# Performance work log

Measured on AMD Instinct MI355X. Metric: run time of the kernel, lower is better.

Reference implementation:

```python
import jax, jax.numpy as jnp
import numpy as np

NEG = -1e18


def _split_heads(x, h):
    # [B, L, D] -> [B, H, L, D/H]
    b, l, d = x.shape
    return x.reshape(b, l, h, d // h).transpose(0, 2, 1, 3)


def _merge_heads(x):
    # [B, H, L, Dh] -> [B, L, H*Dh]
    b, h, l, dh = x.shape
    return x.transpose(0, 2, 1, 3).reshape(b, l, h * dh)


def _sparse(att, dp_map):
    # att: [B, H, L] per-token scores; dp_map: [B, 2, L] (row, col) tree indices.
    # scatter att[b,h,t] -> S[b, h, dp_map[b,0,t], dp_map[b,1,t]], then symmetrize.
    B, H, L = att.shape
    bi = jnp.arange(B)[:, None, None]          # [B,1,1]
    hi = jnp.arange(H)[None, :, None]          # [1,H,1]
    p0 = dp_map[:, 0, :][:, None, :]           # [B,1,L]
    p1 = dp_map[:, 1, :][:, None, :]           # [B,1,L]
    s = jnp.zeros((B, H, L, L), att.dtype)
    s = s.at[bi, hi, p0, p1].set(att)          # matches torch index_put_ (overwrite)
    return s + jnp.swapaxes(s, 2, 3)


def _reverse(values, dp_map):
    # r[b, j] = values[b, dp_map[b,0,j]] for j >= 1; r[b,0] = 0
    idx = dp_map[:, 0, :]                      # [B, L]
    r = jnp.take_along_axis(values, idx[:, :, None], axis=1)
    return r.at[:, 0, :].set(0.0)


def setup_inputs() -> dict:
    key = jax.random.key(0)
    ks = jax.random.split(key, 16)
    B, L, D, R, H = 16, 384, 768, 768, 12
    inp = {
        "queries":   jax.random.normal(ks[0], (B, L, D), jnp.float32),
        "keys":      jax.random.normal(ks[1], (B, L, D), jnp.float32),
        "values":    jax.random.normal(ks[2], (B, L, D), jnp.float32),
        "relations": jax.random.normal(ks[3], (B, L, R), jnp.float32),
        "dp_map":    jax.random.randint(ks[4], (B, 2, L), 0, L, jnp.int32),
        "mask":      jax.random.bernoulli(ks[5], 0.1, (B, L, L)),
        "rel_mask":  jax.random.bernoulli(ks[6], 0.1, (B, L, 1)),
        "Wq":  jax.random.normal(ks[7],  (D, D), jnp.float32) * 0.02,
        "Wk":  jax.random.normal(ks[8],  (D, D), jnp.float32) * 0.02,
        "Wv":  jax.random.normal(ks[9],  (D, D), jnp.float32) * 0.02,
        "Wo":  jax.random.normal(ks[10], (D, D), jnp.float32) * 0.02,
        "Wge": jax.random.normal(ks[11], (D, R), jnp.float32) * 0.02,
        "Wgr": jax.random.normal(ks[12], (R, R), jnp.float32) * 0.02,
        "Vr":  jax.random.normal(ks[13], (R, 1), jnp.float32) * 0.02,
        "Vg":  jax.random.normal(ks[14], (R, 1), jnp.float32) * 0.02,
    }
    return inp


def reference(queries, keys, values, relations, dp_map, mask, rel_mask,
              Wq, Wk, Wv, Wo, Wge, Wgr, Vr, Vg):
    H = 12
    R = Vg.shape[0]
    Dk = Wq.shape[1]
    scale = (Dk // H) ** -0.5

    # config.is_reverse = True path
    hv = jnp.where(rel_mask, 0.0, _reverse(values, dp_map))       # [B,L,D]
    rel = jnp.where(rel_mask, 0.0, relations)                     # [B,L,R]

    # semantic gated mechanism
    rv_h = _split_heads(rel @ Wgr, H)                             # [B,H,L,R/H]
    hs_h = _split_heads(hv @ Wge, H)
    Vg_h = Vg.reshape(H, R // H, 1)
    g = jnp.tanh(jnp.einsum('bhld,hdo->bhlo', hs_h + rv_h, Vg_h))[..., 0]
    gated = _sparse(g, dp_map)                                    # [B,H,L,L]

    q = _split_heads(queries @ Wq, H) * scale
    k = _split_heads(keys @ Wk, H)
    v = _split_heads(values @ Wv, H)
    rel_h = _split_heads(rel, H)
    Vr_h = Vr.reshape(H, R // H, 1)

    self_logits = jnp.einsum('bhqd,bhkd->bhqk', q, k)             # [B,H,L,L]
    rel_logits = _sparse(jnp.einsum('bhld,hdo->bhlo', rel_h, Vr_h)[..., 0], dp_map)

    m = mask[:, None]                                             # [B,1,L,L]
    self_logits = jnp.where(m, NEG, self_logits)
    rel_logits = jnp.where(m, NEG, rel_logits)

    attention_weights = self_logits.sum(axis=1) / H               # [B,L,L]
    sw = jax.nn.softmax(self_logits, axis=-1)
    rw = jax.nn.softmax(rel_logits, axis=-1)
    w = (1.0 - gated) * sw + gated * rw                           # dropout p=0

    ctx = jnp.einsum('bhqk,bhkd->bhqd', w, v)
    out = _merge_heads(ctx) @ Wo
    return out, attention_weights
```

## Files before the change

kernel.cpp:

```cpp
#include <hip/hip_runtime.h>
#include <math.h>

#define Bn 16
#define Lq 384
#define Hn 12
#define Dm 768
#define DH 64
#define QT2 16
#define NEGV (-1e18f)
#define SPADU 404

typedef __attribute__((ext_vector_type(4))) float f32x4;
typedef __attribute__((ext_vector_type(8))) __bf16 bf16x8;
typedef __attribute__((ext_vector_type(4))) __bf16 bf16x4;
typedef unsigned short ushort_t;
typedef unsigned int uint_t;

__device__ __forceinline__ ushort_t f2b(float f) {
  unsigned int u = __float_as_uint(f);
  unsigned int r = (u + 0x7FFFu + ((u >> 16) & 1u)) >> 16;
  return (ushort_t)r;
}
__device__ __forceinline__ float b2f(ushort_t u) {
  return __uint_as_float(((unsigned int)u) << 16);
}
__device__ __forceinline__ bf16x8 cvt8(float4 a, float4 b) {
  bf16x8 r;
  r[0] = (__bf16)a.x; r[1] = (__bf16)a.y; r[2] = (__bf16)a.z; r[3] = (__bf16)a.w;
  r[4] = (__bf16)b.x; r[5] = (__bf16)b.y; r[6] = (__bf16)b.z; r[7] = (__bf16)b.w;
  return r;
}

__global__ __launch_bounds__(256) void k_prep(
    const float* __restrict__ Wge, const float* __restrict__ Wgr,
    const float* __restrict__ Vg,
    float* __restrict__ Age, float* __restrict__ Agr,
    const float* __restrict__ W0, const float* __restrict__ W1,
    const float* __restrict__ W2, const float* __restrict__ W3,
    ushort_t* __restrict__ T0, ushort_t* __restrict__ T1,
    ushort_t* __restrict__ T2, ushort_t* __restrict__ T3,
    const int* __restrict__ dp, int* __restrict__ win)
{
  __shared__ float vg[DH];
  __shared__ float t[32][33];
  int blk = blockIdx.x;
  if (blk < 24) {
    int which = blk / Hn;
    int h = blk % Hn;
    const float* Wsrc = which ? Wgr : Wge;
    float* dst = which ? Agr : Age;
    if (threadIdx.x < DH) vg[threadIdx.x] = Vg[h*DH + threadIdx.x];
    __syncthreads();
    for (int d = threadIdx.x; d < Dm; d += 256) {
      const float* wrow = Wsrc + (size_t)d*Dm + h*DH;
      float s = 0.f;
      #pragma unroll 8
      for (int j = 0; j < DH; ++j) s = fmaf(wrow[j], vg[j], s);
      dst[h*Dm + d] = s;
    }
  } else if (blk < 24 + 2304) {
    int b2 = blk - 24;
    int z = b2 / 576, rem = b2 % 576;
    const float* W = (z == 0) ? W0 : (z == 1) ? W1 : (z == 2) ? W2 : W3;
    ushort_t* WT = (z == 0) ? T0 : (z == 1) ? T1 : (z == 2) ? T2 : T3;
    int k0 = (rem / 24)*32, n0 = (rem % 24)*32;
    int tx = threadIdx.x & 31, ty = threadIdx.x >> 5;
    #pragma unroll
    for (int r = 0; r < 4; ++r)
      t[ty + r*8][tx] = W[(size_t)(k0 + ty + r*8)*Dm + n0 + tx];
    __syncthreads();
    #pragma unroll
    for (int r = 0; r < 4; ++r)
      WT[(size_t)(n0 + ty + r*8)*Dm + k0 + tx] = f2b(t[tx][ty + r*8]);
  } else {
    int i = (blk - 2328)*256 + threadIdx.x;
    int b = i / Lq, l = i % Lq;
    int p0 = dp[(size_t)(b*2+0)*Lq + l];
    int p1 = dp[(size_t)(b*2+1)*Lq + l];
    atomicMax(&win[(size_t)b*Lq*Lq + (size_t)p0*Lq + p1], l);
  }
}

__global__ __launch_bounds__(256) void k_pair(
    const int* __restrict__ win, const int* __restrict__ mask,
    uint_t* __restrict__ wpair)
{
  __shared__ int tB[32][33];
  int b = blockIdx.z;
  int i0 = blockIdx.x*32, j0 = blockIdx.y*32;
  const int* wb = win + (size_t)b*Lq*Lq;
  const int* mb = mask + (size_t)b*Lq*Lq;
  int tx = threadIdx.x & 31, ty = threadIdx.x >> 5;
  #pragma unroll
  for (int rr = 0; rr < 4; ++rr) {
    int r = ty + rr*8;
    tB[r][tx] = wb[(size_t)(j0+r)*Lq + i0 + tx];
  }
  __syncthreads();
  #pragma unroll
  for (int rr = 0; rr < 4; ++rr) {
    int ti = ty + rr*8;
    int i = i0 + ti, j = j0 + tx;
    int l1 = wb[(size_t)i*Lq + j];
    int l2 = tB[tx][ti];
    int mk = mb[(size_t)i*Lq + j];
    wpair[(size_t)b*Lq*Lq + (size_t)i*Lq + j] =
        ((uint_t)(mk != 0) << 31) | ((unsigned)(l1 + 1) << 16) | (unsigned)(l2 + 1);
  }
}

__global__ __launch_bounds__(256) void k_grlog(
    const float* __restrict__ values, const float* __restrict__ relations,
    const int* __restrict__ dp, const int* __restrict__ rel_mask,
    const float* __restrict__ Age, const float* __restrict__ Agr,
    const float* __restrict__ Vr,
    float* __restrict__ g, float* __restrict__ rlog)
{
  int blk = blockIdx.x;
  int b = blk / (Lq/4), l0 = (blk % (Lq/4))*4;
  int tid = threadIdx.x, lane = tid & 63, wave = tid >> 6;
  __shared__ float relrow[4][Dm], hvrow[4][Dm];
  #pragma unroll
  for (int rr = 0; rr < 4; ++rr) {
    int l = l0 + rr;
    int rm = rel_mask[(size_t)b*Lq + l];
    int idx = dp[(size_t)(b*2)*Lq + l];
    const float* vrow = values + ((size_t)b*Lq + idx)*Dm;
    const float* rrow = relations + ((size_t)b*Lq + l)*Dm;
    for (int d = tid; d < Dm; d += 256) {
      relrow[rr][d] = rm ? 0.f : rrow[d];
      hvrow[rr][d]  = (rm || l == 0) ? 0.f : vrow[d];
    }
  }
  __syncthreads();
  int l = l0 + wave;
  for (int h = 0; h < Hn; ++h) {
    float p = 0.f;
    #pragma unroll
    for (int k = 0; k < Dm/64; ++k) {
      int d = lane + 64*k;
      p = fmaf(hvrow[wave][d], Age[h*Dm + d],
          fmaf(relrow[wave][d], Agr[h*Dm + d], p));
    }
    #pragma unroll
    for (int o = 32; o > 0; o >>= 1) p += __shfl_xor(p, o);
    if (lane == 0) g[((size_t)b*Hn + h)*Lq + l] = tanhf(p);
  }
  if (lane < Hn) {
    float s = 0.f;
    #pragma unroll 8
    for (int j = 0; j < DH; ++j)
      s = fmaf(relrow[wave][lane*DH + j], Vr[lane*DH + j], s);
    rlog[((size_t)b*Hn + lane)*Lq + l] = s;
  }
}

__global__ __launch_bounds__(256) void k_mmqkv(
    const float* __restrict__ Xq, const float* __restrict__ Xk,
    const float* __restrict__ Xv,
    const ushort_t* __restrict__ WqT, const ushort_t* __restrict__ WkT,
    const ushort_t* __restrict__ WvT,
    ushort_t* __restrict__ qbf, ushort_t* __restrict__ kbf,
    ushort_t* __restrict__ vTbf)
{
  const int K = Dm;
  __shared__ ushort_t As[128*64];
  __shared__ ushort_t Bs[128*64];

  int z = blockIdx.z;
  const float* A     = (z == 0) ? Xq : (z == 1) ? Xk : Xv;
  const ushort_t* BT = (z == 0) ? WqT : (z == 1) ? WkT : WvT;

  int bm = blockIdx.x;
  int bn = blockIdx.y;
  int m_blk = bm*128;

  int t = threadIdx.x;
  int wave = t >> 6, lane = t & 63;
  int wr = wave >> 1, wc = wave & 1;
  int lrow = lane & 15, lkg = lane >> 4;

  f32x4 acc[4][4];
  #pragma unroll
  for (int i = 0; i < 4; ++i)
    #pragma unroll
    for (int j = 0; j < 4; ++j) acc[i][j] = (f32x4)(0.f);

  int sr = t >> 3, sc8 = t & 7;
  for (int k0 = 0; k0 < K; k0 += 64) {
    __syncthreads();
    #pragma unroll
    for (int i = 0; i < 4; ++i) {
      int row = sr + i*32;
      const float* ap = A + (size_t)(m_blk + row)*K + k0 + sc8*8;
      float4 f0 = *(const float4*)ap;
      float4 f1 = *(const float4*)(ap + 4);
      uint4 vb = *(const uint4*)(BT + (size_t)(bn*128 + row)*K + k0 + sc8*8);
      int slot = sc8 ^ (row & 7);
      *(bf16x8*)&As[row*64 + slot*8] = cvt8(f0, f1);
      *(uint4*)&Bs[row*64 + slot*8] = vb;
    }
    __syncthreads();
    #pragma unroll
    for (int kk = 0; kk < 2; ++kk) {
      bf16x8 aF[4], bF[4];
      int chunk = kk*4 + lkg;
      #pragma unroll
      for (int mi = 0; mi < 4; ++mi) {
        int arow = wr*64 + mi*16 + lrow;
        aF[mi] = *(const bf16x8*)&As[arow*64 + ((chunk ^ (arow & 7)) << 3)];
        int brow = wc*64 + mi*16 + lrow;
        bF[mi] = *(const bf16x8*)&Bs[brow*64 + ((chunk ^ (brow & 7)) << 3)];
      }
      #pragma unroll
      for (int mi = 0; mi < 4; ++mi)
        #pragma unroll
        for (int ni = 0; ni < 4; ++ni)
          acc[mi][ni] = __builtin_amdgcn_mfma_f32_16x16x32_bf16(
              aF[mi], bF[ni], acc[mi][ni], 0, 0, 0);
    }
  }

  float alpha = (z == 0) ? 0.125f : 1.f;
  #pragma unroll
  for (int mi = 0; mi < 4; ++mi) {
    #pragma unroll
    for (int ni = 0; ni < 4; ++ni) {
      f32x4 a = acc[mi][ni];
      int rit = wr*64 + mi*16 + 4*lkg;
      int cit = wc*64 + ni*16 + lrow;
      int gcol = bn*128 + cit;
      if (z < 2) {
        ushort_t* Cb = z ? kbf : qbf;
        int grow = m_blk + rit;
        #pragma unroll
        for (int r = 0; r < 4; ++r)
          Cb[(size_t)(grow + r)*Dm + gcol] = f2b(a[r]*alpha);
      } else {
        int b = bm/3;
        int rl = (bm%3)*128 + rit;
        ushort4 u;
        u.x = f2b(a[0]); u.y = f2b(a[1]); u.z = f2b(a[2]); u.w = f2b(a[3]);
        *(ushort4*)&vTbf[((size_t)b*Dm + gcol)*Lq + rl] = u;
      }
    }
  }
}

template<int MODE>
__global__ __launch_bounds__(256) void k_mm64(
    const ushort_t* __restrict__ A, const ushort_t* __restrict__ BT,
    float* __restrict__ Cf, const int* __restrict__ mask, float alpha)
{
  const int K = Dm;
  __shared__ ushort_t As[64*64];
  __shared__ ushort_t Bs[128*64];

  int bm = blockIdx.x, bn = blockIdx.y, b = blockIdx.z;
  const ushort_t* Ab = (MODE == 3) ? A  + (size_t)b*Lq*Dm : A;
  const ushort_t* Bb = (MODE == 3) ? BT + (size_t)b*Lq*Dm : BT;
  int m0 = bm*64, n0 = bn*128;

  int t = threadIdx.x;
  int wave = t >> 6, lane = t & 63;
  int wr = wave >> 1, wc = wave & 1;
  int lrow = lane & 15, lkg = lane >> 4;

  f32x4 acc[2][4];
  #pragma unroll
  for (int i = 0; i < 2; ++i)
    #pragma unroll
    for (int j = 0; j < 4; ++j) acc[i][j] = (f32x4)(0.f);

  int sr = t >> 3, sc8 = t & 7;
  for (int k0 = 0; k0 < K; k0 += 64) {
    __syncthreads();
    #pragma unroll
    for (int i = 0; i < 2; ++i) {
      int row = sr + i*32;
      uint4 va = *(const uint4*)(Ab + (size_t)(m0 + row)*K + k0 + sc8*8);
      int slot = sc8 ^ (row & 7);
      *(uint4*)&As[row*64 + slot*8] = va;
    }
    #pragma unroll
    for (int i = 0; i < 4; ++i) {
      int row = sr + i*32;
      uint4 vb = *(const uint4*)(Bb + (size_t)(n0 + row)*K + k0 + sc8*8);
      int slot = sc8 ^ (row & 7);
      *(uint4*)&Bs[row*64 + slot*8] = vb;
    }
    __syncthreads();
    #pragma unroll
    for (int kk = 0; kk < 2; ++kk) {
      bf16x8 aF[2], bF[4];
      int chunk = kk*4 + lkg;
      #pragma unroll
      for (int mi = 0; mi < 2; ++mi) {
        int arow = wr*32 + mi*16 + lrow;
        aF[mi] = *(const bf16x8*)&As[arow*64 + ((chunk ^ (arow & 7)) << 3)];
      }
      #pragma unroll
      for (int ni = 0; ni < 4; ++ni) {
        int brow = wc*64 + ni*16 + lrow;
        bF[ni] = *(const bf16x8*)&Bs[brow*64 + ((chunk ^ (brow & 7)) << 3)];
      }
      #pragma unroll
      for (int mi = 0; mi < 2; ++mi)
        #pragma unroll
        for (int ni = 0; ni < 4; ++ni)
          acc[mi][ni] = __builtin_amdgcn_mfma_f32_16x16x32_bf16(
              aF[mi], bF[ni], acc[mi][ni], 0, 0, 0);
    }
  }

  #pragma unroll
  for (int mi = 0; mi < 2; ++mi) {
    #pragma unroll
    for (int ni = 0; ni < 4; ++ni) {
      f32x4 a = acc[mi][ni];
      int rit = wr*32 + mi*16 + 4*lkg;
      int cit = wc*64 + ni*16 + lrow;
      if (MODE == 0) {
        int grow = m0 + rit, gcol = n0 + cit;
        #pragma unroll
        for (int r = 0; r < 4; ++r)
          Cf[(size_t)(grow + r)*Dm + gcol] = a[r]*alpha;
      } else {
        int rl = m0 + rit, cl = n0 + cit;
        const int* mb2 = mask + (size_t)b*Lq*Lq;
        float* awb = Cf + (size_t)b*Lq*Lq;
        #pragma unroll
        for (int r = 0; r < 4; ++r) {
          int m = mb2[(size_t)(rl + r)*Lq + cl];
          awb[(size_t)(rl + r)*Lq + cl] = m ? NEGV : a[r]*alpha;
        }
      }
    }
  }
}

__global__ __launch_bounds__(256, 8) void k_attn3(
    const ushort_t* __restrict__ qbf, const ushort_t* __restrict__ kbf,
    const ushort_t* __restrict__ vT, const uint_t* __restrict__ wpair,
    const float* __restrict__ g, const float* __restrict__ rlog,
    ushort_t* __restrict__ ctxbf)
{
  __shared__ ushort_t S16[QT2][SPADU];
  __shared__ float2 rg2[Lq + 1];

  int bid = blockIdx.x;
  int h  = bid % Hn;
  int qt = (bid / Hn) % (Lq/QT2);
  int b  = bid / (Hn * (Lq/QT2));
  int q0 = qt * QT2;
  int tid = threadIdx.x, lane = tid & 63, wave = tid >> 6;
  int lrow = lane & 15, lkg = lane >> 4;
  int w4 = wave*4;

  const uint_t* wpb = wpair + (size_t)b*Lq*Lq;
  const float* gh = g    + ((size_t)b*Hn + h)*Lq;
  const float* rh = rlog + ((size_t)b*Hn + h)*Lq;

  uint_t wpre[4][6];
  #pragma unroll
  for (int r = 0; r < 4; ++r) {
    const uint_t* wrow = wpb + (size_t)(q0 + w4 + r)*Lq + lane;
    #pragma unroll
    for (int u = 0; u < 6; ++u) wpre[r][u] = wrow[u*64];
  }

  if (tid == 0) { rg2[0].x = 0.f; rg2[0].y = 0.f; }
  for (int e = tid; e < Lq; e += 256) {
    float2 v2; v2.x = rh[e]; v2.y = gh[e];
    rg2[e + 1] = v2;
  }

  {
    const ushort_t* qb = qbf + ((size_t)b*Lq + q0 + lrow)*Dm + h*DH + lkg*8;
    bf16x8 aF0 = *(const bf16x8*)(qb);
    bf16x8 aF1 = *(const bf16x8*)(qb + 32);
    int col0 = wave*96;
    #pragma unroll
    for (int tt = 0; tt < 6; ++tt) {
      int col = col0 + tt*16 + lrow;
      const ushort_t* kb = kbf + ((size_t)b*Lq + col)*Dm + h*DH + lkg*8;
      bf16x8 bF0 = *(const bf16x8*)(kb);
      bf16x8 bF1 = *(const bf16x8*)(kb + 32);
      f32x4 z = (f32x4)(0.f);
      z = __builtin_amdgcn_mfma_f32_16x16x32_bf16(aF0, bF0, z, 0, 0, 0);
      z = __builtin_amdgcn_mfma_f32_16x16x32_bf16(aF1, bF1, z, 0, 0, 0);
      #pragma unroll
      for (int r = 0; r < 4; ++r)
        S16[4*lkg + r][col] = f2b(__expf(z[r]));
    }
  }
  __syncthreads();

  for (int r = 0; r < 4; ++r) {
    int row = w4 + r;
    float sv[6], rv[6], gv[6];
    float ssum = 0.f, rsum = 0.f;
    #pragma unroll
    for (int u = 0; u < 6; ++u) {
      int kj = u*64 + lane;
      uint_t w = wpre[r][u];
      uint_t i1 = (w >> 16) & 0x7FFFu;
      uint_t i2 = w & 0xFFFFu;
      float2 a = rg2[i1];
      float2 c = rg2[i2];
      bool msk = (int)w < 0;
      sv[u] = msk ? 0.f : b2f(S16[row][kj]);
      rv[u] = msk ? 0.f : __expf(a.x + c.x);
      gv[u] = a.y + c.y;
      ssum += sv[u]; rsum += rv[u];
    }
    #pragma unroll
    for (int o = 32; o > 0; o >>= 1) {
      ssum += __shfl_xor(ssum, o);
      rsum += __shfl_xor(rsum, o);
    }
    float si = 1.f/ssum, ri = 1.f/rsum;
    ushort_t* prow = &S16[row][0];
    #pragma unroll
    for (int u = 0; u < 6; ++u) {
      int kj = u*64 + lane;
      float t1 = sv[u]*si;
      float p = fmaf(gv[u], fmaf(rv[u], ri, -t1), t1);
      prow[kj] = f2b(p);
    }
  }
  __syncthreads();

  {
    int dcol = h*DH + wave*16 + lrow;
    const ushort_t* vb = vT + ((size_t)b*Dm + dcol)*Lq + lkg*8;
    const ushort_t* prow = &S16[lrow][0];
    f32x4 o = (f32x4)(0.f);
    #pragma unroll
    for (int ks = 0; ks < 12; ++ks) {
      bf16x4 lo = *(const bf16x4*)(prow + ks*32 + lkg*8);
      bf16x4 hi = *(const bf16x4*)(prow + ks*32 + lkg*8 + 4);
      bf16x8 pa = __builtin_shufflevector(lo, hi, 0,1,2,3,4,5,6,7);
      bf16x8 bv = *(const bf16x8*)(vb + ks*32);
      o = __builtin_amdgcn_mfma_f32_16x16x32_bf16(pa, bv, o, 0, 0, 0);
    }
    #pragma unroll
    for (int r = 0; r < 4; ++r)
      ctxbf[((size_t)b*Lq + q0 + 4*lkg + r)*Dm + dcol] = f2b(o[r]);
  }
}

extern "C" void kernel_launch(void* const* d_in, const int* in_sizes, int n_in,
                              void* d_out, int out_size, void* d_ws, size_t ws_size,
                              hipStream_t stream) {
  const float* queries   = (const float*)d_in[0];
  const float* keys      = (const float*)d_in[1];
  const float* values    = (const float*)d_in[2];
  const float* relations = (const float*)d_in[3];
  const int*   dp_map    = (const int*)d_in[4];
  const int*   mask      = (const int*)d_in[5];
  const int*   rel_mask  = (const int*)d_in[6];
  const float* Wq  = (const float*)d_in[7];
  const float* Wk  = (const float*)d_in[8];
  const float* Wv  = (const float*)d_in[9];
  const float* Wo  = (const float*)d_in[10];
  const float* Wge = (const float*)d_in[11];
  const float* Wgr = (const float*)d_in[12];
  const float* Vr  = (const float*)d_in[13];
  const float* Vg  = (const float*)d_in[14];

  float* ws = (float*)d_ws;
  const size_t SZ   = (size_t)Bn*Lq*Dm;
  const size_t WINS = (size_t)Bn*Lq*Lq;
  const size_t GSZ  = (size_t)Bn*Hn*Lq;

  int*   win  = (int*)ws;
  float* g    = ws + WINS;
  float* rlog = g + GSZ;
  float* Age  = rlog + GSZ;
  float* Agr  = Age + (size_t)Hn*Dm;
  uint_t* wpair = (uint_t*)(Agr + (size_t)Hn*Dm);
  ushort_t* p0 = (ushort_t*)(wpair + WINS);
  ushort_t* qbf  = p0;
  ushort_t* kbf  = p0 + SZ;
  ushort_t* vTbf = p0 + 2*SZ;
  ushort_t* ctxbf= p0 + 3*SZ;
  ushort_t* WqT  = p0 + 4*SZ;
  ushort_t* WkT  = WqT + (size_t)Dm*Dm;
  ushort_t* WvT  = WkT + (size_t)Dm*Dm;
  ushort_t* WoT  = WvT + (size_t)Dm*Dm;

  float* outp = (float*)d_out;
  float* awp  = outp + SZ;

  hipMemsetAsync(win, 0xFF, WINS*sizeof(int), stream);
  k_prep<<<2352, 256, 0, stream>>>(Wge, Wgr, Vg, Age, Agr,
                                   Wq, Wk, Wv, Wo, WqT, WkT, WvT, WoT,
                                   dp_map, win);
  k_grlog<<<Bn*Lq/4, 256, 0, stream>>>(values, relations, dp_map, rel_mask,
                                       Age, Agr, Vr, g, rlog);
  k_mmqkv<<<dim3(48, 6, 3), 256, 0, stream>>>(queries, keys, values,
                                              WqT, WkT, WvT, qbf, kbf, vTbf);
  k_pair<<<dim3(Lq/32, Lq/32, Bn), 256, 0, stream>>>(win, mask, wpair);
  k_mm64<3><<<dim3(6, 3, Bn), 256, 0, stream>>>(qbf, kbf, awp, mask, 1.f/12.f);
  k_attn3<<<Bn*(Lq/QT2)*Hn, 256, 0, stream>>>(qbf, kbf, vTbf, wpair, g, rlog,
                                              ctxbf);
  k_mm64<0><<<dim3(96, 6, 1), 256, 0, stream>>>(ctxbf, WoT, outp, nullptr, 1.f);
}
```

Measured before the change: 197.3 us.

## Replace dense pair map with mask bitsets and sparse per-row relation entries

Replaces the dense per-element wpair array, which k_attn3 read for every (q,k) pair, with a 64-bit mask bitset per row plus a compact per-row list of tree-index entries capped at ECAP. The relation softmax sum is computed as the count of unmasked positions plus corrections from the sparse entries, and only those entries get their probabilities patched. This cuts a large global read in the attention kernel and the wpair write. In exchange it adds atomics in the collect pass and silently drops entries if a row has more than ECAP nonzeros.

Result: slower. 226.2 us (+14.7%).

```diff
diff --git a/kernel.cpp b/kernel.cpp
--- a/kernel.cpp
+++ b/kernel.cpp
@@ -9,12 +9,14 @@
 #define QT2 16
 #define NEGV (-1e18f)
 #define SPADU 404
+#define ECAP 32
 
 typedef __attribute__((ext_vector_type(4))) float f32x4;
 typedef __attribute__((ext_vector_type(8))) __bf16 bf16x8;
 typedef __attribute__((ext_vector_type(4))) __bf16 bf16x4;
 typedef unsigned short ushort_t;
 typedef unsigned int uint_t;
+typedef unsigned long long ull_t;
 
 __device__ __forceinline__ ushort_t f2b(float f) {
   unsigned int u = __float_as_uint(f);
@@ -39,7 +41,8 @@
     const float* __restrict__ W2, const float* __restrict__ W3,
     ushort_t* __restrict__ T0, ushort_t* __restrict__ T1,
     ushort_t* __restrict__ T2, ushort_t* __restrict__ T3,
-    const int* __restrict__ dp, int* __restrict__ win)
+    const int* __restrict__ dp, int* __restrict__ win,
+    const int* __restrict__ mask, ull_t* __restrict__ mbits)
 {
   __shared__ float vg[DH];
   __shared__ float t[32][33];
@@ -72,24 +75,39 @@
     #pragma unroll
     for (int r = 0; r < 4; ++r)
       WT[(size_t)(n0 + ty + r*8)*Dm + k0 + tx] = f2b(t[tx][ty + r*8]);
-  } else {
+  } else if (blk < 2352) {
     int i = (blk - 2328)*256 + threadIdx.x;
     int b = i / Lq, l = i % Lq;
     int p0 = dp[(size_t)(b*2+0)*Lq + l];
     int p1 = dp[(size_t)(b*2+1)*Lq + l];
     atomicMax(&win[(size_t)b*Lq*Lq + (size_t)p0*Lq + p1], l);
-  }
-}
-
-__global__ __launch_bounds__(256) void k_pair(
-    const int* __restrict__ win, const int* __restrict__ mask,
-    uint_t* __restrict__ wpair)
+  } else {
+    int rr = blk - 2352;
+    int lane = threadIdx.x & 63, wave = threadIdx.x >> 6;
+    int gi = rr*4 + wave;
+    const int* mrow = mask + (size_t)gi*Lq;
+    ull_t w0 = __ballot(mrow[lane]        != 0);
+    ull_t w1 = __ballot(mrow[lane + 64]   != 0);
+    ull_t w2 = __ballot(mrow[lane + 128]  != 0);
+    ull_t w3 = __ballot(mrow[lane + 192]  != 0);
+    ull_t w4 = __ballot(mrow[lane + 256]  != 0);
+    ull_t w5 = __ballot(mrow[lane + 320]  != 0);
+    if (lane == 0) {
+      ull_t* out = mbits + (size_t)gi*6;
+      out[0] = w0; out[1] = w1; out[2] = w2;
+      out[3] = w3; out[4] = w4; out[5] = w5;
+    }
+  }
+}
+
+__global__ __launch_bounds__(256) void k_collect(
+    const int* __restrict__ win, uint_t* __restrict__ ent,
+    int* __restrict__ rowcnt)
 {
   __shared__ int tB[32][33];
   int b = blockIdx.z;
   int i0 = blockIdx.x*32, j0 = blockIdx.y*32;
   const int* wb = win + (size_t)b*Lq*Lq;
-  const int* mb = mask + (size_t)b*Lq*Lq;
   int tx = threadIdx.x & 31, ty = threadIdx.x >> 5;
   #pragma unroll
   for (int rr = 0; rr < 4; ++rr) {
@@ -103,9 +121,12 @@
     int i = i0 + ti, j = j0 + tx;
     int l1 = wb[(size_t)i*Lq + j];
     int l2 = tB[tx][ti];
-    int mk = mb[(size_t)i*Lq + j];
-    wpair[(size_t)b*Lq*Lq + (size_t)i*Lq + j] =
-        ((uint_t)(mk != 0) << 31) | ((unsigned)(l1 + 1) << 16) | (unsigned)(l2 + 1);
+    if (l1 >= 0 || l2 >= 0) {
+      int slot = atomicAdd(&rowcnt[(size_t)b*Lq + i], 1);
+      if (slot < ECAP)
+        ent[((size_t)b*Lq + i)*ECAP + slot] =
+            (uint_t)j | ((uint_t)(l1 + 1) << 9) | ((uint_t)(l2 + 1) << 19);
+    }
   }
 }
 
@@ -341,12 +362,14 @@
 
 __global__ __launch_bounds__(256, 8) void k_attn3(
     const ushort_t* __restrict__ qbf, const ushort_t* __restrict__ kbf,
-    const ushort_t* __restrict__ vT, const uint_t* __restrict__ wpair,
+    const ushort_t* __restrict__ vT,
+    const ull_t* __restrict__ mbits, const int* __restrict__ rowcnt,
+    const uint_t* __restrict__ ent,
     const float* __restrict__ g, const float* __restrict__ rlog,
     ushort_t* __restrict__ ctxbf)
 {
   __shared__ ushort_t S16[QT2][SPADU];
-  __shared__ float2 rg2[Lq + 1];
+  __shared__ ull_t mb[QT2][6];
 
   int bid = blockIdx.x;
   int h  = bid % Hn;
@@ -357,22 +380,12 @@
   int lrow = lane & 15, lkg = lane >> 4;
   int w4 = wave*4;
 
-  const uint_t* wpb = wpair + (size_t)b*Lq*Lq;
   const float* gh = g    + ((size_t)b*Hn + h)*Lq;
   const float* rh = rlog + ((size_t)b*Hn + h)*Lq;
 
-  uint_t wpre[4][6];
-  #pragma unroll
-  for (int r = 0; r < 4; ++r) {
-    const uint_t* wrow = wpb + (size_t)(q0 + w4 + r)*Lq + lane;
-    #pragma unroll
-    for (int u = 0; u < 6; ++u) wpre[r][u] = wrow[u*64];
-  }
-
-  if (tid == 0) { rg2[0].x = 0.f; rg2[0].y = 0.f; }
-  for (int e = tid; e < Lq; e += 256) {
-    float2 v2; v2.x = rh[e]; v2.y = gh[e];
-    rg2[e + 1] = v2;
+  if (tid < QT2*6) {
+    int r = tid / 6, u = tid % 6;
+    mb[r][u] = mbits[((size_t)b*Lq + q0 + r)*6 + u];
   }
 
   {
@@ -397,36 +410,56 @@
   __syncthreads();
 
   for (int r = 0; r < 4; ++r) {
-    int row = w4 + r;
-    float sv[6], rv[6], gv[6];
-    float ssum = 0.f, rsum = 0.f;
+    int row = w4 + r, i = q0 + row;
+    ull_t mw[6];
+    #pragma unroll
+    for (int u = 0; u < 6; ++u) mw[u] = mb[row][u];
+    float sv[6];
+    float ssum = 0.f;
     #pragma unroll
     for (int u = 0; u < 6; ++u) {
       int kj = u*64 + lane;
-      uint_t w = wpre[r][u];
-      uint_t i1 = (w >> 16) & 0x7FFFu;
-      uint_t i2 = w & 0xFFFFu;
-      float2 a = rg2[i1];
-      float2 c = rg2[i2];
-      bool msk = (int)w < 0;
-      sv[u] = msk ? 0.f : b2f(S16[row][kj]);
-      rv[u] = msk ? 0.f : __expf(a.x + c.x);
-      gv[u] = a.y + c.y;
-      ssum += sv[u]; rsum += rv[u];
-    }
-    #pragma unroll
-    for (int o = 32; o > 0; o >>= 1) {
-      ssum += __shfl_xor(ssum, o);
-      rsum += __shfl_xor(rsum, o);
-    }
+      bool mk = (mw[u] >> lane) & 1ull;
+      sv[u] = mk ? 0.f : b2f(S16[row][kj]);
+      ssum += sv[u];
+    }
+    #pragma unroll
+    for (int o = 32; o > 0; o >>= 1) ssum += __shfl_xor(ssum, o);
+    int nun = 384;
+    #pragma unroll
+    for (int u = 0; u < 6; ++u) nun -= (int)__popcll(mw[u]);
+    int cnt = rowcnt[(size_t)b*Lq + i];
+    cnt = cnt > ECAP ? ECAP : cnt;
+    const uint_t* entrow = ent + ((size_t)b*Lq + i)*ECAP;
+    float rext = 0.f;
+    for (int e = 0; e < cnt; ++e) {
+      uint_t en = entrow[e];
+      int j = en & 511;
+      if ((mb[row][j >> 6] >> (j & 63)) & 1ull) continue;
+      int l1 = (int)((en >> 9) & 1023) - 1;
+      int l2 = (int)(en >> 19) - 1;
+      float rel = 0.f;
+      if (l1 >= 0) rel += rh[l1];
+      if (l2 >= 0) rel += rh[l2];
+      rext += __expf(rel) - 1.f;
+    }
+    float rsum = (float)nun + rext;
     float si = 1.f/ssum, ri = 1.f/rsum;
     ushort_t* prow = &S16[row][0];
     #pragma unroll
-    for (int u = 0; u < 6; ++u) {
-      int kj = u*64 + lane;
-      float t1 = sv[u]*si;
-      float p = fmaf(gv[u], fmaf(rv[u], ri, -t1), t1);
-      prow[kj] = f2b(p);
+    for (int u = 0; u < 6; ++u)
+      prow[u*64 + lane] = f2b(sv[u]*si);
+    for (int e = 0; e < cnt; ++e) {
+      uint_t en = entrow[e];
+      int j = en & 511;
+      if ((mb[row][j >> 6] >> (j & 63)) & 1ull) continue;
+      int l1 = (int)((en >> 9) & 1023) - 1;
+      int l2 = (int)(en >> 19) - 1;
+      float rel = 0.f, gvv = 0.f;
+      if (l1 >= 0) { rel += rh[l1]; gvv += gh[l1]; }
+      if (l2 >= 0) { rel += rh[l2]; gvv += gh[l2]; }
+      float pfix = (1.f - gvv)*b2f(prow[j]) + gvv*__expf(rel)*ri;
+      if (lane == 0) prow[j] = f2b(pfix);
     }
   }
   __syncthreads();
@@ -473,14 +506,17 @@
   const size_t SZ   = (size_t)Bn*Lq*Dm;
   const size_t WINS = (size_t)Bn*Lq*Lq;
   const size_t GSZ  = (size_t)Bn*Hn*Lq;
+  const size_t ROWS = (size_t)Bn*Lq;
 
   int*   win  = (int*)ws;
   float* g    = ws + WINS;
   float* rlog = g + GSZ;
   float* Age  = rlog + GSZ;
   float* Agr  = Age + (size_t)Hn*Dm;
-  uint_t* wpair = (uint_t*)(Agr + (size_t)Hn*Dm);
-  ushort_t* p0 = (ushort_t*)(wpair + WINS);
+  ull_t* mbits = (ull_t*)(Agr + (size_t)Hn*Dm);
+  int*   rowcnt = (int*)(mbits + ROWS*6);
+  uint_t* ent  = (uint_t*)(rowcnt + ROWS);
+  ushort_t* p0 = (ushort_t*)(ent + ROWS*ECAP);
   ushort_t* qbf  = p0;
   ushort_t* kbf  = p0 + SZ;
   ushort_t* vTbf = p0 + 2*SZ;
@@ -494,16 +530,17 @@
   float* awp  = outp + SZ;
 
   hipMemsetAsync(win, 0xFF, WINS*sizeof(int), stream);
-  k_prep<<<2352, 256, 0, stream>>>(Wge, Wgr, Vg, Age, Agr,
+  hipMemsetAsync(rowcnt, 0, ROWS*sizeof(int), stream);
+  k_prep<<<3888, 256, 0, stream>>>(Wge, Wgr, Vg, Age, Agr,
                                    Wq, Wk, Wv, Wo, WqT, WkT, WvT, WoT,
-                                   dp_map, win);
+                                   dp_map, win, mask, mbits);
   k_grlog<<<Bn*Lq/4, 256, 0, stream>>>(values, relations, dp_map, rel_mask,
                                        Age, Agr, Vr, g, rlog);
   k_mmqkv<<<dim3(48, 6, 3), 256, 0, stream>>>(queries, keys, values,
                                               WqT, WkT, WvT, qbf, kbf, vTbf);
-  k_pair<<<dim3(Lq/32, Lq/32, Bn), 256, 0, stream>>>(win, mask, wpair);
+  k_collect<<<dim3(12, 12, Bn), 256, 0, stream>>>(win, ent, rowcnt);
   k_mm64<3><<<dim3(6, 3, Bn), 256, 0, stream>>>(qbf, kbf, awp, mask, 1.f/12.f);
-  k_attn3<<<Bn*(Lq/QT2)*Hn, 256, 0, stream>>>(qbf, kbf, vTbf, wpair, g, rlog,
-                                              ctxbf);
+  k_attn3<<<Bn*(Lq/QT2)*Hn, 256, 0, stream>>>(qbf, kbf, vTbf, mbits, rowcnt,
+                                              ent, g, rlog, ctxbf);
   k_mm64<0><<<dim3(96, 6, 1), 256, 0, stream>>>(ctxbf, WoT, outp, nullptr, 1.f);
 }
```
